# Kernel tuning notes

Hardware: AMD Instinct MI355X
Metric: run time of the kernel (lower is better)

Reference implementation:

```python
import jax, jax.numpy as jnp
import numpy as np

B, L, H, HEADS, DK = 256, 20, 128, 8, 16
NT, NR = 4, 4
CHILD, PARENT = 30001, 500
N1S, N1D, E1 = 50000, 20000, 300000
N2, E2 = 20000, 200000
T = B * L
N4D, E4 = 5000, 150000
EC2P = 8000
D2 = H // 2  # gamma=0.5 split for diachronic embedding


def _ln(x):
    m = jnp.mean(x, -1, keepdims=True)
    v = jnp.var(x, -1, keepdims=True)
    return (x - m) * jax.lax.rsqrt(v + 1e-5)


def _tmod(h, w, b):
    # temporal modulation with per-node diachronic params (activ='sin')
    return jnp.concatenate([h[..., :D2], h[..., D2:] * jnp.sin(w[..., D2:] + b[..., D2:])], -1)


def _dia(e, w, b, t):
    t = t[..., None].astype(e.dtype)
    return jnp.concatenate([e[..., :D2], e[..., D2:] * jnp.sin(w[..., D2:] * t + b[..., D2:])], -1)


def _typed(x, t, W):
    # type-conditioned linear: W [NT, in, out]; small NT -> compute all, select
    y = jnp.einsum('nh,tho->tno', x, W)
    return y[t, jnp.arange(x.shape[0])]


def _seg_softmax(s, seg, n):
    m = jax.ops.segment_max(s, seg, num_segments=n)
    m = jnp.where(jnp.isfinite(m), m, 0.0)
    ex = jnp.exp(s - m[seg])
    den = jax.ops.segment_sum(ex, seg, num_segments=n)
    return ex / jnp.maximum(den[seg], 1e-9)


def _htgt(src_h, src_t, tw, tb, eh, esrc, edst, etype, dst_h, dst_t, KW, QW, VW, OW, EW, mu):
    # relational multi-head attention on a bipartite block (HTGTLayer, pre_norm)
    nd = dst_h.shape[0]
    hs = _tmod(_ln(src_h), tw, tb)
    k = _typed(hs, src_t, KW).reshape(-1, HEADS, DK)
    v = _typed(hs, src_t, VW).reshape(-1, HEADS, DK)
    q = _typed(_ln(dst_h), dst_t, QW).reshape(nd, HEADS, DK)
    ke = k[esrc] + (eh @ EW).reshape(-1, HEADS, DK)
    score = (q[edst] * ke).sum(-1) * mu[etype] / np.float32(np.sqrt(DK))  # [E, HEADS]
    a = _seg_softmax(score, edst, nd)
    agg = jax.ops.segment_sum(a[..., None] * v[esrc], edst, num_segments=nd).reshape(nd, H)
    return _typed(agg, dst_t, OW) + dst_h


def _lstm(x, Wi, Wh, b):
    h0 = jnp.zeros((x.shape[0], H), x.dtype)
    def step(carry, xt):
        h, c = carry
        g = xt @ Wi + h @ Wh + b
        i, f, gg, o = jnp.split(g, 4, -1)
        c = jax.nn.sigmoid(f) * c + jax.nn.sigmoid(i) * jnp.tanh(gg)
        h = jax.nn.sigmoid(o) * jnp.tanh(c)
        return (h, c), h
    _, hs = jax.lax.scan(step, (h0, h0), jnp.swapaxes(x, 0, 1))
    return jnp.swapaxes(hs, 0, 1)


def _forward(seq, seq_ntype, dur, stime, etime, g1_nid, g1_ntype, g1_esrc, g1_edst, g1_etype, g1_ew,
             g2_src_sel, g2_esrc, g2_edst, g2_etype, g2_ew, tok_sel, g4_esrc, g4_edst, g4_etype, g4_ew,
             pe_p, pe_c, emb, hist_emb, edge_emb, dia_w, dia_b, t2v_w, t2v_b, exp_W, exp_b,
             lstm1_Wi, lstm1_Wh, lstm1_b, lstm2_Wi, lstm2_Wh, lstm2_b,
             convK, convQ, convV, convO, convE, convMu, ipW, iaW, skip):
    # ---- sequence module ----
    e0 = emb[seq]
    st = _dia(e0, dia_w[seq], dia_b[seq], stime)
    et = _dia(e0, dia_w[seq], dia_b[seq], etime)
    t = dur[..., None].astype(jnp.float32)
    tv = jnp.concatenate([t2v_w[:1] * t + t2v_b[:1], jnp.sin(t2v_w[1:] * t + t2v_b[1:])], -1)
    x = jax.nn.relu(jnp.concatenate([st, et, tv], -1) @ exp_W + exp_b)
    h1 = _lstm(x, lstm1_Wi, lstm1_Wh, lstm1_b)
    his = jnp.swapaxes(h1, 0, 1).reshape(T, H)  # packed (time-major) token states
    tok_id = jnp.swapaxes(seq, 0, 1).reshape(T)
    tok_nt = jnp.swapaxes(seq_ntype, 0, 1).reshape(T)
    # ---- conv1 (g2g) on block 1 ----
    sh1 = emb[g1_nid]
    xg = jax.nn.relu(_htgt(sh1, g1_ntype, dia_w[g1_nid], dia_b[g1_nid], edge_emb[g1_ew],
                           g1_esrc, g1_edst, g1_etype, sh1[:N1D], g1_ntype[:N1D],
                           convK[0], convQ[0], convV[0], convO[0], convE[0], convMu[0]))
    # ---- conv2 (g2s): graph nodes -> packed sequence tokens ----
    gnid2 = g1_nid[g2_src_sel]
    dst_h2 = xg[tok_sel] + his
    x2 = jax.nn.relu(_htgt(xg[g2_src_sel], g1_ntype[g2_src_sel], dia_w[gnid2], dia_b[gnid2], edge_emb[g2_ew],
                           g2_esrc, g2_edst, g2_etype, dst_h2, tok_nt,
                           convK[1], convQ[1], convV[1], convO[1], convE[1], convMu[1]))
    seq2 = jnp.swapaxes(x2.reshape(L, B, H), 0, 1)
    h2 = _lstm(seq2, lstm2_Wi, lstm2_Wh, lstm2_b)  # final seq_embed
    # ---- individual pooling (attn) + history push ----
    ent = jnp.swapaxes(h2, 0, 1).reshape(T, H)
    a = _typed(jnp.tanh(_typed(ent, tok_nt, ipW)), tok_nt, iaW)[:, 0]
    w = _seg_softmax(a, tok_id, CHILD)
    node_embed = jax.ops.segment_sum(w[:, None] * ent, tok_id, num_segments=CHILD)
    cnt = jax.ops.segment_sum(jnp.ones((T,), jnp.float32), tok_id, num_segments=CHILD)
    hist2 = jnp.where(cnt[:, None] > 0, node_embed, hist_emb)
    # ---- graph module: conv3, conv4 with skip-gated pull ----
    alpha = jax.nn.sigmoid(skip)[g1_ntype][:, None]
    x0 = emb[g1_nid] * alpha + hist2[g1_nid] * (1.0 - alpha)
    x3 = jax.nn.relu(_htgt(x0, g1_ntype, dia_w[g1_nid], dia_b[g1_nid], edge_emb[g1_ew],
                           g1_esrc, g1_edst, g1_etype, x0[:N1D], g1_ntype[:N1D],
                           convK[2], convQ[2], convV[2], convO[2], convE[2], convMu[2]))
    nid4 = g1_nid[:N1D]
    child_embed = _htgt(x3, g1_ntype[:N1D], dia_w[nid4], dia_b[nid4], edge_emb[g4_ew],
                        g4_esrc, g4_edst, g4_etype, x3[:N4D], g1_ntype[:N4D],
                        convK[3], convQ[3], convV[3], convO[3], convE[3], convMu[3])
    # ---- parent pooling (avg over c2p map) ----
    psum = jax.ops.segment_sum(child_embed[pe_c], pe_p, num_segments=PARENT)
    pcnt = jax.ops.segment_sum(jnp.ones((EC2P,), jnp.float32), pe_p, num_segments=PARENT)
    parent_embed = psum / jnp.maximum(pcnt, 1.0)[:, None]
    return (h2, child_embed, parent_embed)


def setup_inputs() -> dict:
    key = jax.random.key(0)
    ks = iter(jax.random.split(key, 64))
    def ri(shape, hi):
        return jax.random.randint(next(ks), shape, 0, hi, dtype=jnp.int32)
    def rn(shape, s=0.02):
        return jax.random.normal(next(ks), shape, dtype=jnp.float32) * s
    return dict(
        seq=ri((B, L), CHILD), seq_ntype=ri((B, L), NT), dur=ri((B, L), 40),
        stime=ri((B, L), 60), etime=ri((B, L), 60),
        g1_nid=ri((N1S,), CHILD), g1_ntype=ri((N1S,), NT),
        g1_esrc=ri((E1,), N1S), g1_edst=ri((E1,), N1D), g1_etype=ri((E1,), NR), g1_ew=ri((E1,), 50),
        g2_src_sel=ri((N2,), N1D), g2_esrc=ri((E2,), N2), g2_edst=ri((E2,), T),
        g2_etype=ri((E2,), NR), g2_ew=ri((E2,), 50),
        tok_sel=ri((T,), N1D),
        g4_esrc=ri((E4,), N1D), g4_edst=ri((E4,), N4D), g4_etype=ri((E4,), NR), g4_ew=ri((E4,), 50),
        pe_p=ri((EC2P,), PARENT), pe_c=ri((EC2P,), N4D),
        emb=rn((CHILD, H), 0.05), hist_emb=rn((CHILD, H), 0.05), edge_emb=rn((50, 32), 0.05),
        dia_w=rn((CHILD, H), 0.05), dia_b=rn((CHILD, H), 0.05),
        t2v_w=rn((16,), 0.1), t2v_b=rn((16,), 0.1),
        exp_W=rn((2 * H + 16, H)), exp_b=jnp.zeros((H,), jnp.float32),
        lstm1_Wi=rn((H, 4 * H)), lstm1_Wh=rn((H, 4 * H)), lstm1_b=jnp.zeros((4 * H,), jnp.float32),
        lstm2_Wi=rn((H, 4 * H)), lstm2_Wh=rn((H, 4 * H)), lstm2_b=jnp.zeros((4 * H,), jnp.float32),
        convK=rn((4, NT, H, H)), convQ=rn((4, NT, H, H)), convV=rn((4, NT, H, H)), convO=rn((4, NT, H, H)),
        convE=rn((4, 32, H)), convMu=jnp.ones((4, NR, HEADS), jnp.float32),
        ipW=rn((NT, H, H)), iaW=rn((NT, H, 1)), skip=jnp.ones((NT,), jnp.float32),
    )


def reference(seq, seq_ntype, dur, stime, etime, g1_nid, g1_ntype, g1_esrc, g1_edst, g1_etype, g1_ew,
              g2_src_sel, g2_esrc, g2_edst, g2_etype, g2_ew, tok_sel, g4_esrc, g4_edst, g4_etype, g4_ew,
              pe_p, pe_c, emb, hist_emb, edge_emb, dia_w, dia_b, t2v_w, t2v_b, exp_W, exp_b,
              lstm1_Wi, lstm1_Wh, lstm1_b, lstm2_Wi, lstm2_Wh, lstm2_b,
              convK, convQ, convV, convO, convE, convMu, ipW, iaW, skip):
    return _forward(seq, seq_ntype, dur, stime, etime, g1_nid, g1_ntype, g1_esrc, g1_edst, g1_etype, g1_ew,
                    g2_src_sel, g2_esrc, g2_edst, g2_etype, g2_ew, tok_sel, g4_esrc, g4_edst, g4_etype, g4_ew,
                    pe_p, pe_c, emb, hist_emb, edge_emb, dia_w, dia_b, t2v_w, t2v_b, exp_W, exp_b,
                    lstm1_Wi, lstm1_Wh, lstm1_b, lstm2_Wi, lstm2_Wh, lstm2_b,
                    convK, convQ, convV, convO, convE, convMu, ipW, iaW, skip)
```

## Files before the change

kernel.cpp:

```cpp
#include <hip/hip_runtime.h>
#include <math.h>

#define BB 256
#define LL 20
#define HH 128
#define NH 8
#define D2C 64
#define NTY 4
#define NRL 4
#define CHILDN 30001
#define PARENTN 500
#define N1SN 50000
#define N1DN 20000
#define E1N 300000
#define N2N 20000
#define E2N 200000
#define TT (BB*LL)
#define N4DN 5000
#define E4N 150000
#define EC2PN 8000

typedef __attribute__((ext_vector_type(8))) short bfrag;
typedef __attribute__((ext_vector_type(4))) float ffrag;

__device__ __forceinline__ unsigned fenc(float f){ unsigned u=__float_as_uint(f); return (u&0x80000000u)? ~u : (u|0x80000000u); }
__device__ __forceinline__ float fdec(unsigned u){ return (u&0x80000000u)? __uint_as_float(u^0x80000000u) : __uint_as_float(~u); }
__device__ __forceinline__ float sigfast(float x){ return 1.f/(1.f+__expf(-x)); }
__device__ __forceinline__ float tanhfast(float x){ float e = __expf(-2.f*x); return (1.f-e)/(1.f+e); }
__device__ __forceinline__ short f2bf(float f){
  unsigned u = __float_as_uint(f);
  unsigned r = u + 0x7FFFu + ((u>>16)&1u);
  return (short)(r>>16);
}

__global__ void k_init(float* hist2, float* cnt, unsigned* amax, float* aden,
                       float* psum, float* pcnt, int* cntall,
                       int* icnt1, int* icnt2, int* icnt3){
  int i = blockIdx.x*256 + threadIdx.x;
  if(i < CHILDN*HH) hist2[i] = 0.f;
  if(i < CHILDN){ cnt[i] = 0.f; aden[i] = 0.f; amax[i] = 0x007FFFFFu; }
  if(i < PARENTN*HH) psum[i] = 0.f;
  if(i < PARENTN) pcnt[i] = 0.f;
  if(i < 5*NTY) cntall[i] = 0;
  if(i < N1DN) icnt1[i] = 0;
  if(i < TT)   icnt2[i] = 0;
  if(i < N4DN) icnt3[i] = 0;
}

__global__ void k_sindia(const float* __restrict__ dia_w, const float* __restrict__ dia_b,
                         float* __restrict__ sdia){
  int i = blockIdx.x*256 + threadIdx.x;
  if(i >= CHILDN*64) return;
  int c = i >> 6, k = (i & 63) + 64;
  sdia[i] = __sinf(dia_w[(size_t)c*HH+k] + dia_b[(size_t)c*HH+k]);
}

__global__ __launch_bounds__(512) void k_featx2(const int* __restrict__ seq, const int* __restrict__ dur,
                        const int* __restrict__ stime, const int* __restrict__ etime,
                        const float* __restrict__ emb, const float* __restrict__ dia_w, const float* __restrict__ dia_b,
                        const float* __restrict__ t2v_w, const float* __restrict__ t2v_b,
                        const float* __restrict__ exp_W, const float* __restrict__ exp_b, float* __restrict__ xout){
  __shared__ float feat[32*273];
  int base = blockIdx.x*32;
  int j = threadIdx.x >> 4;
  int p = threadIdx.x & 15;
  int row = base + j;
  int node = seq[row];
  float ts = (float)stime[row], te = (float)etime[row];
  const float* ep = emb + (size_t)node*HH;
  float* fr = feat + j*273;
  int o0 = p*8;
  #pragma unroll
  for(int ii=0; ii<8; ii+=4){
    int o = o0 + ii;
    float4 e = *(const float4*)(ep + o);
    float4 st = e, et = e;
    if(o >= D2C){
      float4 w = *(const float4*)(dia_w + (size_t)node*HH + o);
      float4 b = *(const float4*)(dia_b + (size_t)node*HH + o);
      st.x = e.x*__sinf(w.x*ts+b.x); st.y = e.y*__sinf(w.y*ts+b.y);
      st.z = e.z*__sinf(w.z*ts+b.z); st.w = e.w*__sinf(w.w*ts+b.w);
      et.x = e.x*__sinf(w.x*te+b.x); et.y = e.y*__sinf(w.y*te+b.y);
      et.z = e.z*__sinf(w.z*te+b.z); et.w = e.w*__sinf(w.w*te+b.w);
    }
    fr[o] = st.x; fr[o+1] = st.y; fr[o+2] = st.z; fr[o+3] = st.w;
    fr[128+o] = et.x; fr[128+o+1] = et.y; fr[128+o+2] = et.z; fr[128+o+3] = et.w;
  }
  if(p == 0){
    float td = (float)dur[row];
    #pragma unroll
    for(int i=0;i<16;i++){
      float w = t2v_w[i], b = t2v_b[i];
      fr[256+i] = (i==0) ? (w*td + b) : __sinf(w*td + b);
    }
  }
  __syncthreads();
  int oc = (threadIdx.x & 31)*4;
  int jg = threadIdx.x >> 5;
  const float* f0 = feat + (jg*2)*273;
  const float* f1 = feat + (jg*2+1)*273;
  float4 a0 = {0,0,0,0}, a1 = {0,0,0,0};
  for(int k=0;k<272;k++){
    float4 w = *(const float4*)(exp_W + (size_t)k*HH + oc);
// ... 101 lines not shown
  if(threadIdx.x < NTY) h[threadIdx.x] = 0;
  __syncthreads();
  int nt = 0, r = 0;
  bool act = (i < TT);
  if(act){
    int b = i % BB, l = i / BB;
    tokid[i] = seq[b*LL+l];
    nt = seq_nt[b*LL+l];
    toknt[i] = nt;
    r = atomicAdd(&h[nt], 1);
  }
  __syncthreads();
  if(threadIdx.x < NTY && h[threadIdx.x] > 0)
    bs[threadIdx.x] = atomicAdd(&cnts[threadIdx.x], h[threadIdx.x]);
  __syncthreads();
  if(act) idxb[nt*TT + bs[nt] + r] = i;
}

__global__ void k_prep2scat(const int* __restrict__ sel, const int* __restrict__ g1_nid,
                            const int* __restrict__ g1_nt, int* __restrict__ gnid2,
                            int* __restrict__ cnts, int* __restrict__ idxb){
  __shared__ int h[NTY];
  __shared__ int bs[NTY];
  int i = blockIdx.x*256 + threadIdx.x;
  if(threadIdx.x < NTY) h[threadIdx.x] = 0;
  __syncthreads();
  int nt = 0, r = 0;
  bool act = (i < N2N);
  if(act){
    int s = sel[i];
    gnid2[i] = g1_nid[s];
    nt = g1_nt[s];
    r = atomicAdd(&h[nt], 1);
  }
  __syncthreads();
  if(threadIdx.x < NTY && h[threadIdx.x] > 0)
    bs[threadIdx.x] = atomicAdd(&cnts[threadIdx.x], h[threadIdx.x]);
  __syncthreads();
  if(act) idxb[nt*N2N + bs[nt] + r] = i;
}

__global__ void k_dst2(const int* tok_sel, const float* xg, const float* h1, float* dst2){
  int t = blockIdx.x; int o = threadIdx.x;
  int b = t % BB, l = t / BB;
  dst2[t*HH+o] = xg[tok_sel[t]*HH+o] + h1[(b*LL+l)*HH+o];
}

__global__ void k_x0(const int* nid, const int* ntype, const float* emb, const float* hist2,
                     const float* skip, float* srcbuf){
  int i = blockIdx.x; int o = threadIdx.x;
  float a = sigfast(skip[ntype[i]]);
  int nd = nid[i];
  srcbuf[i*HH+o] = emb[nd*HH+o]*a + hist2[nd*HH+o]*(1.f-a);
}

__global__ void k_scatter3(const int* __restrict__ types,
                           int* cnts1, int* idx1, int* cnts2, int* idx2, int* cnts3, int* idx3){
  __shared__ int h[3][NTY];
  __shared__ int bs[3][NTY];
  int i = blockIdx.x*256 + threadIdx.x;
  if(threadIdx.x < 3*NTY) (&h[0][0])[threadIdx.x] = 0;
  __syncthreads();
  int t = 0, r1 = 0, r2 = 0, r3 = 0;
  bool a1 = (i < N1SN), a2 = (i < N1DN), a3 = (i < N4DN);
  if(a1){
    t = types[i];
    r1 = atomicAdd(&h[0][t], 1);
    if(a2) r2 = atomicAdd(&h[1][t], 1);
    if(a3) r3 = atomicAdd(&h[2][t], 1);
  }
  __syncthreads();
  if(threadIdx.x < NTY){
    int ty = threadIdx.x;
    if(h[0][ty] > 0) bs[0][ty] = atomicAdd(&cnts1[ty], h[0][ty]);
    if(h[1][ty] > 0) bs[1][ty] = atomicAdd(&cnts2[ty], h[1][ty]);
    if(h[2][ty] > 0) bs[2][ty] = atomicAdd(&cnts3[ty], h[2][ty]);
  }
  __syncthreads();
  if(a1) idx1[t*N1SN + bs[0][t] + r1] = i;
  if(a2) idx2[t*N1DN + bs[1][t] + r2] = i;
  if(a3) idx3[t*N4DN + bs[2][t] + r3] = i;
}

__global__ void k_prepack(const float* convK, const float* convV, const float* convQ,
                          const float* convO, short* Wsw){
  int m = blockIdx.x;
  int fam = m >> 4;
  int lt = m & 15;
  const float* src = (fam==0?convK:fam==1?convV:fam==2?convQ:convO) + (size_t)lt*HH*HH;
  short* dst = Wsw + (size_t)m*16384;
  for(int s=0;s<64;s++){
    int i = threadIdx.x + 256*s;
    int j = i & 7, lane = (i>>3)&63, kc = (i>>9)&3, nt = i>>11;
    int k = kc*32 + (lane>>4)*8 + j;
    int n = nt*16 + (lane&15);
    dst[i] = f2bf(src[k*HH+n]);
  }
}

__global__ __launch_bounds__(256) void k_gemm_kvq(
    const float* __restrict__ Xs, const int* __restrict__ src_nid, const int* __restrict__ smap,
    const float* __restrict__ sdia,
    const int* __restrict__ idxs, const int* __restrict__ cnts_s, int stride_s,
    const bfrag* __restrict__ WK, const bfrag* __restrict__ WV, unsigned* __restrict__ KVp,
    const float* __restrict__ Xq, const int* __restrict__ qmap,
    const int* __restrict__ idxd, const int* __restrict__ cnts_d, int stride_d,
    const bfrag* __restrict__ WQ, float* __restrict__ Qbuf){
  __shared__ float xs[32*132];
  __shared__ float red[512];
  __shared__ float mean_s[32], inv_s[32];
  __shared__ int sid[32], nid[32], xrow[32];
  int t = blockIdx.y;
  int tid = threadIdx.x;
  int base = blockIdx.x * 32;
  if(blockIdx.z == 0){
    int cnt = cnts_s[t];
    if(base >= cnt || cnt == 0) return;
    int nn = min(32, cnt - base);
    const int* ids = idxs + (size_t)t*stride_s + base;
    if(tid < 32){
      int s_ = (tid < nn) ? ids[tid] : ids[0];
      sid[tid] = s_; nid[tid] = src_nid[s_];
      xrow[tid] = smap ? smap[s_] : s_;
    }
    __syncthreads();
    #pragma unroll
    for(int s=0;s<16;s++){
      int elem = tid + 256*s;
      int k = elem & 127, j = elem >> 7;
      xs[j*132 + k] = Xs[(size_t)xrow[j]*HH + k];
    }
    __syncthreads();
    {
      int j = tid >> 3, p = tid & 7;
      float sm=0.f, sq=0.f;
      const float* xr = xs + j*132 + p*16;
      #pragma unroll
      for(int i=0;i<16;i++){ float v = xr[i]; sm += v; sq += v*v; }
      red[j*8+p] = sm; red[256 + j*8+p] = sq;
    }
    __syncthreads();
    if(tid < 32){
      float sm=0.f, sq=0.f;
      #pragma unroll
      for(int p=0;p<8;p++){ sm += red[tid*8+p]; sq += red[256+tid*8+p]; }
      float mean = sm*(1.f/128.f);
      float var = sq*(1.f/128.f) - mean*mean;
      mean_s[tid] = mean;
      inv_s[tid] = 1.f/sqrtf(fmaxf(var,0.f)+1e-5f);
    }
    __syncthreads();
    #pragma unroll
    for(int s=0;s<16;s++){
      int elem = tid + 256*s;
      int k = elem & 127, j = elem >> 7;
      float v = (xs[j*132+k] - mean_s[j]) * inv_s[j];
      if(k >= D2C) v *= sdia[(size_t)nid[j]*64 + (k - D2C)];
      xs[j*132+k] = v;
    }
    __syncthreads();
    int lane = tid & 63, w = tid >> 6;
    int mt = w & 1, ng0 = (w>>1)*4;
    int arow = mt*16 + (lane & 15);
    int koff = (lane >> 4)*8;
    int tb = t*2048;
    ffrag aK[4], aV[4];
    #pragma unroll
    for(int i=0;i<4;i++){ aK[i] = (ffrag){0.f,0.f,0.f,0.f}; aV[i] = (ffrag){0.f,0.f,0.f,0.f}; }
    #pragma unroll
    for(int kc=0;kc<4;kc++){
      const float* ap = xs + arow*132 + kc*32 + koff;
      bfrag a;
      #pragma unroll
      for(int j=0;j<8;j++) a[j] = f2bf(ap[j]);
      #pragma unroll
      for(int nt=0;nt<4;nt++){
        int fi = tb + ((ng0+nt)*4 + kc)*64 + lane;
        bfrag bk = WK[fi];
        bfrag bv = WV[fi];
        aK[nt] = __builtin_amdgcn_mfma_f32_16x16x32_bf16(a, bk, aK[nt], 0, 0, 0);
        aV[nt] = __builtin_amdgcn_mfma_f32_16x16x32_bf16(a, bv, aV[nt], 0, 0, 0);
      }
    }
    int col0 = lane & 15;
    int rb = mt*16 + (lane>>4)*4;
    #pragma unroll
    for(int nt=0;nt<4;nt++){
      int col = (ng0+nt)*16 + col0;
      #pragma unroll
      for(int i=0;i<4;i++){
        int n = rb + i;
        if(n < nn){
          unsigned pk = (unsigned short)f2bf(aK[nt][i]);
          unsigned pv = (unsigned short)f2bf(aV[nt][i]);
          KVp[(size_t)sid[n]*HH + col] = (pv<<16) | pk;
        }
      }
    }
  } else {
    int cnt = cnts_d[t];
    if(base >= cnt || cnt == 0) return;
    int nn = min(32, cnt - base);
    const int* ids = idxd + (size_t)t*stride_d + base;
    if(tid < 32){
      int s_ = (tid < nn) ? ids[tid] : ids[0];
      sid[tid] = s_;
      xrow[tid] = qmap ? qmap[s_] : s_;
    }
    __syncthreads();
    #pragma unroll
    for(int s=0;s<16;s++){
      int elem = tid + 256*s;
      int k = elem & 127, j = elem >> 7;
      xs[j*132 + k] = Xq[(size_t)xrow[j]*HH + k];
    }
    __syncthreads();
    {
      int j = tid >> 3, p = tid & 7;
      float sm=0.f, sq=0.f;
      const float* xr = xs + j*132 + p*16;
      #pragma unroll
      for(int i=0;i<16;i++){ float v = xr[i]; sm += v; sq += v*v; }
      red[j*8+p] = sm; red[256 + j*8+p] = sq;
    }
    __syncthreads();
    if(tid < 32){
      float sm=0.f, sq=0.f;
      #pragma unroll
      for(int p=0;p<8;p++){ sm += red[tid*8+p]; sq += red[256+tid*8+p]; }
      float mean = sm*(1.f/128.f);
      float var = sq*(1.f/128.f) - mean*mean;
      mean_s[tid] = mean;
      inv_s[tid] = 1.f/sqrtf(fmaxf(var,0.f)+1e-5f);
    }
    __syncthreads();
    #pragma unroll
    for(int s=0;s<16;s++){
      int elem = tid + 256*s;
      int k = elem & 127, j = elem >> 7;
      xs[j*132+k] = (xs[j*132+k] - mean_s[j]) * inv_s[j];
    }
    __syncthreads();
    int lane = tid & 63, w = tid >> 6;
    int mt = w & 1, ng0 = (w>>1)*4;
    int arow = mt*16 + (lane & 15);
    int koff = (lane >> 4)*8;
    int tb = t*2048;
    ffrag acc[4];
    #pragma unroll
    for(int i=0;i<4;i++) acc[i] = (ffrag){0.f,0.f,0.f,0.f};
    #pragma unroll
    for(int kc=0;kc<4;kc++){
      const float* ap = xs + arow*132 + kc*32 + koff;
      bfrag a;
      #pragma unroll
      for(int j=0;j<8;j++) a[j] = f2bf(ap[j]);
      #pragma unroll
      for(int nt=0;nt<4;nt++){
        bfrag b = WQ[tb + ((ng0+nt)*4 + kc)*64 + lane];
        acc[nt] = __builtin_amdgcn_mfma_f32_16x16x32_bf16(a, b, acc[nt], 0, 0, 0);
      }
    }
    int col0 = lane & 15;
    int rb = mt*16 + (lane>>4)*4;
    #pragma unroll
    for(int nt=0;nt<4;nt++){
      int col = (ng0+nt)*16 + col0;
      #pragma unroll
      for(int i=0;i<4;i++){
        int n = rb + i;
        if(n < nn) Qbuf[(size_t)sid[n]*HH + col] = acc[nt][i];
      }
    }
  }
}

__global__ void k_gemm_t5(const float* X, const int* xmap, const int* idxb, const int* cnts, int stride,
                          const bfrag* W, const float* resid, const int* rmap, float* Y, float* Y2,
                          int relu){
  int t = blockIdx.y;
  int cnt = cnts[t];
  int base = blockIdx.x * 32;
  if(base >= cnt || cnt == 0) return;
  int nn = min(32, cnt - base);
  const int* ids = idxb + (size_t)t*stride + base;
  __shared__ float xs[32*132];
  __shared__ int sid[32], xrow[32], rrow[32];
  int tid = threadIdx.x;
  if(tid < 32){
    int s_ = (tid < nn) ? ids[tid] : ids[0];
    sid[tid] = s_;
    xrow[tid] = xmap ? xmap[s_] : s_;
    rrow[tid] = rmap ? rmap[s_] : s_;
  }
  __syncthreads();
  #pragma unroll
  for(int s=0;s<16;s++){
    int elem = tid + 256*s;
    int k = elem & 127, j = elem >> 7;
    xs[j*132 + k] = X[(size_t)xrow[j]*HH + k];
  }
  __syncthreads();
  int lane = tid & 63, w = tid >> 6;
  int mt = w & 1, ng0 = (w>>1)*4;
  int arow = mt*16 + (lane & 15);
  int koff = (lane >> 4)*8;
  int tb = t*2048;
  ffrag acc[4];
  #pragma unroll
  for(int i=0;i<4;i++) acc[i] = (ffrag){0.f,0.f,0.f,0.f};
  #pragma unroll
  for(int kc=0;kc<4;kc++){
    const float* ap = xs + arow*132 + kc*32 + koff;
    bfrag a;
    #pragma unroll
    for(int j=0;j<8;j++) a[j] = f2bf(ap[j]);
    #pragma unroll
    for(int nt=0;nt<4;nt++){
      bfrag b = W[tb + ((ng0+nt)*4 + kc)*64 + lane];
      acc[nt] = __builtin_amdgcn_mfma_f32_16x16x32_bf16(a, b, acc[nt], 0, 0, 0);
    }
  }
  int col0 = lane & 15;
  int rb = mt*16 + (lane>>4)*4;
  #pragma unroll
  for(int nt=0;nt<4;nt++){
    int col = (ng0+nt)*16 + col0;
    #pragma unroll
    for(int i=0;i<4;i++){
      int n = rb + i;
      if(n < nn){
        size_t r = (size_t)sid[n]*HH + col;
        float v = acc[nt][i];
        if(resid){
          v += resid[(size_t)rrow[n]*HH + col];
          if(relu) v = fmaxf(v, 0.f);
        }
        Y[r] = v;
        if(Y2) Y2[r] = v;
      }
    }
  }
}

__global__ void k_edge_tab4(const float* edge_emb, const float* convE, float* EW2all){
  int r = blockIdx.x; int layer = blockIdx.y; int o = threadIdx.x;
  const float* EWp = convE + (size_t)layer*32*HH;
  float acc = 0.f;
  for(int j=0;j<32;j++) acc += edge_emb[r*32+j]*EWp[j*HH+o];
  EW2all[((size_t)layer*50 + r)*HH + o] = acc;
}

__global__ void k_hist_dst(const int* edst, int E, int* cnt){
  int e = blockIdx.x*256 + threadIdx.x;
  if(e < E) atomicAdd(&cnt[edst[e]], 1);
}
__global__ void k_scan3(const int* c1, int n1, int* r1, int* u1,
                        const int* c2, int n2, int* r2, int* u2,
                        const int* c3, int n3, int* r3, int* u3){
  __shared__ int tsum[1024];
  const int* cnt; int n; int* row_ptr; int* cursor;
  if(blockIdx.x == 0){ cnt=c1; n=n1; row_ptr=r1; cursor=u1; }
  else if(blockIdx.x == 1){ cnt=c2; n=n2; row_ptr=r2; cursor=u2; }
  else { cnt=c3; n=n3; row_ptr=r3; cursor=u3; }
  int tid = threadIdx.x;
  int per = (n + 1023) / 1024;
  int start = tid*per; int end = min(start+per, n);
  int s = 0;
  for(int i=start;i<end;i++) s += cnt[i];
  tsum[tid] = s; __syncthreads();
  for(int off=1;off<1024;off<<=1){
    int v = (tid>=off) ? tsum[tid-off] : 0;
    __syncthreads();
    tsum[tid] += v;
    __syncthreads();
  }
  int run = (tid==0) ? 0 : tsum[tid-1];
  for(int i=start;i<end;i++){ row_ptr[i]=run; cursor[i]=run; run += cnt[i]; }
  if(end == n) row_ptr[n] = run;
}
__global__ void k_fillperm(const int* edst, const int* esrc, const int* ew, const int* ety,
                           int E, int* cursor, int2* meta){
  int e = blockIdx.x*256 + threadIdx.x;
// ... 149 lines not shown
                              hipStream_t stream){
  const int* seq     = (const int*)d_in[0];
  const int* seq_nt  = (const int*)d_in[1];
  const int* dur     = (const int*)d_in[2];
  const int* stime   = (const int*)d_in[3];
  const int* etime   = (const int*)d_in[4];
  const int* g1_nid  = (const int*)d_in[5];
  const int* g1_nt   = (const int*)d_in[6];
  const int* g1_esrc = (const int*)d_in[7];
  const int* g1_edst = (const int*)d_in[8];
  const int* g1_ety  = (const int*)d_in[9];
  const int* g1_ew   = (const int*)d_in[10];
  const int* g2_sel  = (const int*)d_in[11];
  const int* g2_esrc = (const int*)d_in[12];
  const int* g2_edst = (const int*)d_in[13];
  const int* g2_ety  = (const int*)d_in[14];
  const int* g2_ew   = (const int*)d_in[15];
  const int* tok_sel = (const int*)d_in[16];
  const int* g4_esrc = (const int*)d_in[17];
  const int* g4_edst = (const int*)d_in[18];
  const int* g4_ety  = (const int*)d_in[19];
  const int* g4_ew   = (const int*)d_in[20];
  const int* pe_p    = (const int*)d_in[21];
  const int* pe_c    = (const int*)d_in[22];
  const float* emb     = (const float*)d_in[23];
  const float* hist_emb= (const float*)d_in[24];
  const float* edge_emb= (const float*)d_in[25];
  const float* dia_w   = (const float*)d_in[26];
  const float* dia_b   = (const float*)d_in[27];
  const float* t2v_w   = (const float*)d_in[28];
  const float* t2v_b   = (const float*)d_in[29];
  const float* exp_W   = (const float*)d_in[30];
  const float* exp_b   = (const float*)d_in[31];
  const float* l1Wi    = (const float*)d_in[32];
  const float* l1Wh    = (const float*)d_in[33];
  const float* l1b     = (const float*)d_in[34];
  const float* l2Wi    = (const float*)d_in[35];
  const float* l2Wh    = (const float*)d_in[36];
  const float* l2b     = (const float*)d_in[37];
  const float* convK   = (const float*)d_in[38];
  const float* convQ   = (const float*)d_in[39];
  const float* convV   = (const float*)d_in[40];
  const float* convO   = (const float*)d_in[41];
  const float* convE   = (const float*)d_in[42];
  const float* convMu  = (const float*)d_in[43];
  const float* ipW     = (const float*)d_in[44];
  const float* iaW     = (const float*)d_in[45];
  const float* skip    = (const float*)d_in[46];
  float* outp = (float*)d_out;

  char* wsp = (char*)d_ws;
  size_t off = 0;
  auto A = [&](size_t nbytes)->char*{ char* p = wsp+off; off += (nbytes+255)&~(size_t)255; return p; };
  float*    srcbuf = (float*)   A((size_t)N1SN*HH*4);
  unsigned* KVp    = (unsigned*)A((size_t)N1SN*HH*4);
  float*    Qbuf   = (float*)   A((size_t)N1DN*HH*4);
  float*    Abuf   = (float*)   A((size_t)N1DN*HH*4);
  float*    xbuf   = (float*)   A((size_t)TT*HH*4);
  float*    gpre   = (float*)   A((size_t)TT*512*4);
  float*    h1     = (float*)   A((size_t)TT*HH*4);
  float*    dst2   = (float*)   A((size_t)TT*HH*4);
  float*    xg     = (float*)   A((size_t)N1DN*HH*4);
  float*    x2     = (float*)   A((size_t)TT*HH*4);
  float*    h2f    = (float*)   A((size_t)TT*HH*4);
  float*    hist2  = (float*)   A((size_t)CHILDN*HH*4);
  float*    cnt    = (float*)   A((size_t)CHILDN*4);
  float*    abuf   = (float*)   A((size_t)TT*4);
  unsigned* amax   = (unsigned*)A((size_t)CHILDN*4);
  float*    aden   = (float*)   A((size_t)CHILDN*4);
  float*    x3     = (float*)   A((size_t)N1DN*HH*4);
  float*    cef    = (float*)   A((size_t)N4DN*HH*4);
  float*    psum   = (float*)   A((size_t)PARENTN*HH*4);
  float*    pcnt   = (float*)   A((size_t)PARENTN*4);
  float*    sdia   = (float*)   A((size_t)CHILDN*64*4);
  int*      tokid  = (int*)     A((size_t)TT*4);
  int*      toknt  = (int*)     A((size_t)TT*4);
  int*      gnid2  = (int*)     A((size_t)N2N*4);
  int*      idxS1  = (int*)     A((size_t)NTY*N1SN*4);
  int*      idxS2  = (int*)     A((size_t)NTY*N1DN*4);
  int*      idxS3  = (int*)     A((size_t)NTY*N2N*4);
  int*      idxS4  = (int*)     A((size_t)NTY*TT*4);
  int*      idxS5  = (int*)     A((size_t)NTY*N4DN*4);
  int*      cntall = (int*)     A((size_t)5*NTY*4);
  float*    EW2all = (float*)   A((size_t)4*50*HH*4);
  short*    Wsw    = (short*)   A((size_t)64*16384*2);
  int*      g1row  = (int*)     A((size_t)(N1DN+1)*4);
  int2*     g1meta = (int2*)    A((size_t)E1N*8);
  int*      g2row  = (int*)     A((size_t)(TT+1)*4);
  int2*     g2meta = (int2*)    A((size_t)E2N*8);
  int*      g4row  = (int*)     A((size_t)(N4DN+1)*4);
  int2*     g4meta = (int2*)    A((size_t)E4N*8);
  int*      icnt1  = (int*)     A((size_t)(N1DN+1)*4);
  int*      icur1  = (int*)     A((size_t)(N1DN+1)*4);
  int*      icnt2  = (int*)     A((size_t)(TT+1)*4);
  int*      icur2  = (int*)     A((size_t)(TT+1)*4);
  int*      icnt3  = (int*)     A((size_t)(N4DN+1)*4);
  int*      icur3  = (int*)     A((size_t)(N4DN+1)*4);
  if(off > ws_size) return;

  auto run_conv = [&](const float* src_X, const int* src_nid, const int* srcmap, int nsrc,
                      const int* idx_src, int* cnt_src, int stride_src,
                      const float* q_X, const int* q_map,
                      const float* resid_X, const int* r_map, int ndst,
                      const int* idx_dst, int* cnt_dst, int stride_dst,
                      const int* rowp, const int2* meta,
                      int layer, float* outbuf, float* out2, int relu){
    const bfrag* WB = (const bfrag*)Wsw;
    const bfrag* WK = WB + (size_t)( 0 + layer*4)*2048;
    const bfrag* WV = WB + (size_t)(16 + layer*4)*2048;
    const bfrag* WQ = WB + (size_t)(32 + layer*4)*2048;
    const bfrag* WO = WB + (size_t)(48 + layer*4)*2048;
    const float* MU  = convMu + (size_t)layer*NRL*NH;
    const float* EW2 = EW2all + (size_t)layer*50*HH;
    int gx = max((nsrc+31)/32, (ndst+31)/32);
    dim3 gkvq(gx, NTY, 2);
    k_gemm_kvq<<<gkvq, 256, 0, stream>>>(src_X, src_nid, srcmap, sdia,
                                         idx_src, cnt_src, stride_src, WK, WV, KVp,
                                         q_X, q_map, idx_dst, cnt_dst, stride_dst, WQ, Qbuf);
    k_attn_fused8<<<ndst, HH, 0, stream>>>(rowp, meta, KVp, Qbuf, EW2, MU, Abuf);
    dim3 gq((ndst+31)/32, NTY);
    k_gemm_t5<<<gq, 256, 0, stream>>>(Abuf, (const int*)nullptr, idx_dst, cnt_dst, stride_dst, WO,
                                      resid_X, r_map, outbuf, out2, relu);
  };

  k_init<<<(CHILDN*HH+255)/256, 256, 0, stream>>>(hist2, cnt, amax, aden, psum, pcnt, cntall,
                                                  icnt1, icnt2, icnt3);
  k_sindia<<<(CHILDN*64+255)/256, 256, 0, stream>>>(dia_w, dia_b, sdia);
  k_prepack<<<64, 256, 0, stream>>>(convK, convV, convQ, convO, Wsw);
  k_edge_tab4<<<dim3(50,4), HH, 0, stream>>>(edge_emb, convE, EW2all);
  k_scatter3<<<(N1SN+255)/256, 256, 0, stream>>>(g1_nt, cntall+0*NTY, idxS1,
                                                 cntall+1*NTY, idxS2, cntall+4*NTY, idxS5);
  k_tokprep<<<(TT+255)/256, 256, 0, stream>>>(seq, seq_nt, tokid, toknt, cntall+3*NTY, idxS4);
  k_prep2scat<<<(N2N+255)/256, 256, 0, stream>>>(g2_sel, g1_nid, g1_nt, gnid2, cntall+2*NTY, idxS3);
  k_hist_dst<<<(E1N+255)/256, 256, 0, stream>>>(g1_edst, E1N, icnt1);
  k_hist_dst<<<(E2N+255)/256, 256, 0, stream>>>(g2_edst, E2N, icnt2);
  k_hist_dst<<<(E4N+255)/256, 256, 0, stream>>>(g4_edst, E4N, icnt3);
  k_scan3<<<3, 1024, 0, stream>>>(icnt1, N1DN, g1row, icur1,
                                  icnt2, TT,   g2row, icur2,
                                  icnt3, N4DN, g4row, icur3);
  k_fillperm<<<(E1N+255)/256, 256, 0, stream>>>(g1_edst, g1_esrc, g1_ew, g1_ety, E1N, icur1, g1meta);
  k_fillperm<<<(E2N+255)/256, 256, 0, stream>>>(g2_edst, g2_esrc, g2_ew, g2_ety, E2N, icur2, g2meta);
  k_fillperm<<<(E4N+255)/256, 256, 0, stream>>>(g4_edst, g4_esrc, g4_ew, g4_ety, E4N, icur3, g4meta);

  k_featx2<<<TT/32, 512, 0, stream>>>(seq, dur, stime, etime, emb, dia_w, dia_b, t2v_w, t2v_b, exp_W, exp_b, xbuf);
  k_xwi2<<<(TT+15)/16, 256, 0, stream>>>(xbuf, l1Wi, l1b, gpre, TT, 0);
  k_lstm_fused<<<BB, 512, 0, stream>>>(gpre, l1Wh, h1, (float*)nullptr);

  run_conv(emb, g1_nid, g1_nid, N1SN, idxS1, cntall+0*NTY, N1SN,
           emb, g1_nid,
           emb, g1_nid, N1DN, idxS2, cntall+1*NTY, N1DN,
           g1row, g1meta, 0, xg, (float*)nullptr, 1);

  k_dst2<<<TT, HH, 0, stream>>>(tok_sel, xg, h1, dst2);
  run_conv(xg, gnid2, g2_sel, N2N, idxS3, cntall+2*NTY, N2N,
           dst2, (const int*)nullptr,
           dst2, (const int*)nullptr, TT, idxS4, cntall+3*NTY, TT,
           g2row, g2meta, 1, x2, (float*)nullptr, 1);

  k_xwi2<<<(TT+15)/16, 256, 0, stream>>>(x2, l2Wi, l2b, gpre, TT, 1);
  k_lstm_fused<<<BB, 512, 0, stream>>>(gpre, l2Wh, h2f, outp);

  k_tokatt<<<TT, HH, 0, stream>>>(h2f, toknt, ipW, iaW, abuf, amax, tokid);
  k_tokexp<<<(TT+255)/256, 256, 0, stream>>>(tokid, abuf, amax, aden, cnt);
  k_tokagg<<<TT, HH, 0, stream>>>(tokid, abuf, aden, h2f, hist2);
  k_histfix<<<CHILDN, HH, 0, stream>>>(cnt, hist_emb, hist2);

  k_x0<<<N1SN, HH, 0, stream>>>(g1_nid, g1_nt, emb, hist2, skip, srcbuf);
  run_conv(srcbuf, g1_nid, (const int*)nullptr, N1SN, idxS1, cntall+0*NTY, N1SN,
           srcbuf, (const int*)nullptr,
           srcbuf, (const int*)nullptr, N1DN, idxS2, cntall+1*NTY, N1DN,
           g1row, g1meta, 2, x3, (float*)nullptr, 1);

  run_conv(x3, g1_nid, (const int*)nullptr, N1DN, idxS2, cntall+1*NTY, N1DN,
           x3, (const int*)nullptr,
           x3, (const int*)nullptr, N4DN, idxS5, cntall+4*NTY, N4DN,
           g4row, g4meta, 3, cef, outp + (size_t)TT*HH, 0);

  k_peagg<<<EC2PN, HH, 0, stream>>>(pe_p, pe_c, cef, psum, pcnt);
  k_parent<<<PARENTN, HH, 0, stream>>>(psum, pcnt, outp + (size_t)TT*HH + (size_t)N4DN*HH);
}
```

Before: 777.2 us.

## Compact typed GEMM grids with precomputed tile descriptors and vectorised loads

Adds a single-block kernel that builds a compact list of 32-row tile descriptors per conv configuration from the per-type counts. The KVQ and output GEMMs then launch exactly over those tiles instead of a max-sized grid per type with many early-exit blocks. The change also merges the K/V and Q code paths, replaces the shared-memory layernorm reduction with wave shuffles, and uses float4 row gathers. The cost is an extra tiny serial launch and a descriptor indirection in each block.

```diff
diff --git a/kernel.cpp b/kernel.cpp
--- a/kernel.cpp
+++ b/kernel.cpp
@@ -19,6 +19,7 @@
 #define N4DN 5000
 #define E4N 150000
 #define EC2PN 8000
+#define TDSTRIDE 2304
 
 typedef __attribute__((ext_vector_type(8))) short bfrag;
 typedef __attribute__((ext_vector_type(4))) float ffrag;
@@ -286,6 +287,40 @@
   if(a3) idx3[t*N4DN + bs[2][t] + r3] = i;
 }
 
+__global__ void k_mktiles(const int* __restrict__ cntall, int* __restrict__ tdesc, int* __restrict__ tcnt){
+  __shared__ int start[3][2][NTY];
+  if(threadIdx.x == 0){
+    const int srcg[3] = {0,2,1};
+    const int dstg[3] = {1,3,4};
+    for(int c=0;c<3;c++){
+      int acc = 0;
+      for(int z=0;z<2;z++){
+        int g = (z==0) ? srcg[c] : dstg[c];
+        int zacc = 0;
+        for(int t=0;t<NTY;t++){
+          start[c][z][t] = acc;
+          int tiles = (cntall[g*NTY+t]+31)>>5;
+          acc += tiles; zacc += tiles;
+        }
+        tcnt[c*2+z] = zacc;
+      }
+    }
+  }
+  __syncthreads();
+  const int srcg[3] = {0,2,1};
+  const int dstg[3] = {1,3,4};
+  for(int c=0;c<3;c++){
+    for(int z=0;z<2;z++){
+      int g = (z==0) ? srcg[c] : dstg[c];
+      for(int t=0;t<NTY;t++){
+        int tiles = (cntall[g*NTY+t]+31)>>5;
+        for(int i=threadIdx.x; i<tiles; i+=blockDim.x)
+          tdesc[c*TDSTRIDE + start[c][z][t] + i] = (int)(((unsigned)z<<31) | ((unsigned)t<<28) | (unsigned)(i<<5));
+      }
+    }
+  }
+}
+
 __global__ void k_prepack(const float* convK, const float* convV, const float* convQ,
                           const float* convO, short* Wsw){
   int m = blockIdx.x;
@@ -303,6 +338,7 @@
 }
 
 __global__ __launch_bounds__(256) void k_gemm_kvq(
+    const int* __restrict__ tdesc, const int* __restrict__ tcnt,
     const float* __restrict__ Xs, const int* __restrict__ src_nid, const int* __restrict__ smap,
     const float* __restrict__ sdia,
     const int* __restrict__ idxs, const int* __restrict__ cnts_s, int stride_s,
@@ -311,49 +347,55 @@
     const int* __restrict__ idxd, const int* __restrict__ cnts_d, int stride_d,
     const bfrag* __restrict__ WQ, float* __restrict__ Qbuf){
   __shared__ float xs[32*132];
-  __shared__ float red[512];
   __shared__ float mean_s[32], inv_s[32];
   __shared__ int sid[32], nid[32], xrow[32];
-  int t = blockIdx.y;
+  int ntk = tcnt[0], ntq = tcnt[1];
+  int bid = blockIdx.x;
+  if(bid >= ntk + ntq) return;
+  unsigned ud = (unsigned)tdesc[bid];
+  int isQ = ud >> 31;
+  int t = (ud >> 28) & 7;
+  int base = ud & 0x0FFFFFFF;
   int tid = threadIdx.x;
-  int base = blockIdx.x * 32;
-  if(blockIdx.z == 0){
-    int cnt = cnts_s[t];
-    if(base >= cnt || cnt == 0) return;
-    int nn = min(32, cnt - base);
-    const int* ids = idxs + (size_t)t*stride_s + base;
-    if(tid < 32){
-      int s_ = (tid < nn) ? ids[tid] : ids[0];
-      sid[tid] = s_; nid[tid] = src_nid[s_];
-      xrow[tid] = smap ? smap[s_] : s_;
-    }
-    __syncthreads();
-    #pragma unroll
-    for(int s=0;s<16;s++){
-      int elem = tid + 256*s;
-      int k = elem & 127, j = elem >> 7;
-      xs[j*132 + k] = Xs[(size_t)xrow[j]*HH + k];
-    }
-    __syncthreads();
-    {
-      int j = tid >> 3, p = tid & 7;
-      float sm=0.f, sq=0.f;
-      const float* xr = xs + j*132 + p*16;
-      #pragma unroll
-      for(int i=0;i<16;i++){ float v = xr[i]; sm += v; sq += v*v; }
-      red[j*8+p] = sm; red[256 + j*8+p] = sq;
-    }
-    __syncthreads();
-    if(tid < 32){
-      float sm=0.f, sq=0.f;
-      #pragma unroll
-      for(int p=0;p<8;p++){ sm += red[tid*8+p]; sq += red[256+tid*8+p]; }
+  int cnt = isQ ? cnts_d[t] : cnts_s[t];
+  if(base >= cnt) return;
+  int nn = min(32, cnt - base);
+  const float* X = isQ ? Xq : Xs;
+  const int* map = isQ ? qmap : smap;
+  const int* ids = (isQ ? idxd + (size_t)t*stride_d : idxs + (size_t)t*stride_s) + base;
+  if(tid < 32){
+    int s_ = (tid < nn) ? ids[tid] : ids[0];
+    sid[tid] = s_;
+    if(!isQ) nid[tid] = src_nid[s_];
+    xrow[tid] = map ? map[s_] : s_;
+  }
+  __syncthreads();
+  #pragma unroll
+  for(int s=0;s<4;s++){
+    int e4 = tid + 256*s;
+    int j = e4 >> 5, c4 = (e4 & 31)*4;
+    *(float4*)&xs[j*132 + c4] = *(const float4*)&X[(size_t)xrow[j]*HH + c4];
+  }
+  __syncthreads();
+  {
+    int wid = tid >> 6, lane = tid & 63;
+    int row = wid*8 + (lane>>3), p = lane & 7;
+    const float* xr = xs + row*132 + p*16;
+    float sm=0.f, sq=0.f;
+    #pragma unroll
+    for(int i=0;i<16;i++){ float v = xr[i]; sm += v; sq += v*v; }
+    sm += __shfl_xor(sm, 1, 64); sq += __shfl_xor(sq, 1, 64);
+    sm += __shfl_xor(sm, 2, 64); sq += __shfl_xor(sq, 2, 64);
+    sm += __shfl_xor(sm, 4, 64); sq += __shfl_xor(sq, 4, 64);
+    if(p == 0){
       float mean = sm*(1.f/128.f);
       float var = sq*(1.f/128.f) - mean*mean;
-      mean_s[tid] = mean;
-      inv_s[tid] = 1.f/sqrtf(fmaxf(var,0.f)+1e-5f);
-    }
-    __syncthreads();
+      mean_s[row] = mean;
+      inv_s[row] = 1.f/sqrtf(fmaxf(var,0.f)+1e-5f);
+    }
+  }
+  __syncthreads();
+  if(!isQ){
     #pragma unroll
     for(int s=0;s<16;s++){
       int elem = tid + 256*s;
@@ -362,12 +404,21 @@
       if(k >= D2C) v *= sdia[(size_t)nid[j]*64 + (k - D2C)];
       xs[j*132+k] = v;
     }
-    __syncthreads();
-    int lane = tid & 63, w = tid >> 6;
-    int mt = w & 1, ng0 = (w>>1)*4;
-    int arow = mt*16 + (lane & 15);
-    int koff = (lane >> 4)*8;
-    int tb = t*2048;
+  } else {
+    #pragma unroll
+    for(int s=0;s<16;s++){
+      int elem = tid + 256*s;
+      int k = elem & 127, j = elem >> 7;
+      xs[j*132+k] = (xs[j*132+k] - mean_s[j]) * inv_s[j];
+    }
+  }
+  __syncthreads();
+  int lane = tid & 63, w = tid >> 6;
+  int mt = w & 1, ng0 = (w>>1)*4;
+  int arow = mt*16 + (lane & 15);
+  int koff = (lane >> 4)*8;
+  int tb = t*2048;
+  if(!isQ){
     ffrag aK[4], aV[4];
     #pragma unroll
     for(int i=0;i<4;i++){ aK[i] = (ffrag){0.f,0.f,0.f,0.f}; aV[i] = (ffrag){0.f,0.f,0.f,0.f}; }
@@ -402,54 +453,6 @@
       }
     }
   } else {
-    int cnt = cnts_d[t];
-    if(base >= cnt || cnt == 0) return;
-    int nn = min(32, cnt - base);
-    const int* ids = idxd + (size_t)t*stride_d + base;
-    if(tid < 32){
-      int s_ = (tid < nn) ? ids[tid] : ids[0];
-      sid[tid] = s_;
-      xrow[tid] = qmap ? qmap[s_] : s_;
-    }
-    __syncthreads();
-    #pragma unroll
-    for(int s=0;s<16;s++){
-      int elem = tid + 256*s;
-      int k = elem & 127, j = elem >> 7;
-      xs[j*132 + k] = Xq[(size_t)xrow[j]*HH + k];
-    }
-    __syncthreads();
-    {
-      int j = tid >> 3, p = tid & 7;
-      float sm=0.f, sq=0.f;
-      const float* xr = xs + j*132 + p*16;
-      #pragma unroll
-      for(int i=0;i<16;i++){ float v = xr[i]; sm += v; sq += v*v; }
-      red[j*8+p] = sm; red[256 + j*8+p] = sq;
-    }
-    __syncthreads();
-    if(tid < 32){
-      float sm=0.f, sq=0.f;
-      #pragma unroll
-      for(int p=0;p<8;p++){ sm += red[tid*8+p]; sq += red[256+tid*8+p]; }
-      float mean = sm*(1.f/128.f);
-      float var = sq*(1.f/128.f) - mean*mean;
-      mean_s[tid] = mean;
-      inv_s[tid] = 1.f/sqrtf(fmaxf(var,0.f)+1e-5f);
-    }
-    __syncthreads();
-    #pragma unroll
-    for(int s=0;s<16;s++){
-      int elem = tid + 256*s;
-      int k = elem & 127, j = elem >> 7;
-      xs[j*132+k] = (xs[j*132+k] - mean_s[j]) * inv_s[j];
-    }
-    __syncthreads();
-    int lane = tid & 63, w = tid >> 6;
-    int mt = w & 1, ng0 = (w>>1)*4;
-    int arow = mt*16 + (lane & 15);
-    int koff = (lane >> 4)*8;
-    int tb = t*2048;
     ffrag acc[4];
     #pragma unroll
     for(int i=0;i<4;i++) acc[i] = (ffrag){0.f,0.f,0.f,0.f};
@@ -479,30 +482,34 @@
   }
 }
 
-__global__ void k_gemm_t5(const float* X, const int* xmap, const int* idxb, const int* cnts, int stride,
-                          const bfrag* W, const float* resid, const int* rmap, float* Y, float* Y2,
-                          int relu){
-  int t = blockIdx.y;
+__global__ __launch_bounds__(256) void k_gemm_t5(
+    const int* __restrict__ tdesc, const int* __restrict__ tcnt,
+    const float* X, const int* idxb, const int* cnts, int stride,
+    const bfrag* W, const float* resid, const int* rmap, float* Y, float* Y2,
+    int relu){
+  __shared__ float xs[32*132];
+  __shared__ int sid[32], rrow[32];
+  int ntk = tcnt[0], ntq = tcnt[1];
+  if(blockIdx.x >= ntq) return;
+  unsigned ud = (unsigned)tdesc[ntk + blockIdx.x];
+  int t = (ud >> 28) & 7;
+  int base = ud & 0x0FFFFFFF;
   int cnt = cnts[t];
-  int base = blockIdx.x * 32;
-  if(base >= cnt || cnt == 0) return;
+  if(base >= cnt) return;
   int nn = min(32, cnt - base);
   const int* ids = idxb + (size_t)t*stride + base;
-  __shared__ float xs[32*132];
-  __shared__ int sid[32], xrow[32], rrow[32];
   int tid = threadIdx.x;
   if(tid < 32){
     int s_ = (tid < nn) ? ids[tid] : ids[0];
     sid[tid] = s_;
-    xrow[tid] = xmap ? xmap[s_] : s_;
     rrow[tid] = rmap ? rmap[s_] : s_;
   }
   __syncthreads();
   #pragma unroll
-  for(int s=0;s<16;s++){
-    int elem = tid + 256*s;
-    int k = elem & 127, j = elem >> 7;
-    xs[j*132 + k] = X[(size_t)xrow[j]*HH + k];
+  for(int s=0;s<4;s++){
+    int e4 = tid + 256*s;
+    int j = e4 >> 5, c4 = (e4 & 31)*4;
+    *(float4*)&xs[j*132 + c4] = *(const float4*)&X[(size_t)sid[j]*HH + c4];
   }
   __syncthreads();
   int lane = tid & 63, w = tid >> 6;
@@ -818,6 +825,8 @@
   int*      idxS4  = (int*)     A((size_t)NTY*TT*4);
   int*      idxS5  = (int*)     A((size_t)NTY*N4DN*4);
   int*      cntall = (int*)     A((size_t)5*NTY*4);
+  int*      tdesc  = (int*)     A((size_t)3*TDSTRIDE*4);
+  int*      tcnt   = (int*)     A((size_t)8*4);
   float*    EW2all = (float*)   A((size_t)4*50*HH*4);
   short*    Wsw    = (short*)   A((size_t)64*16384*2);
   int*      g1row  = (int*)     A((size_t)(N1DN+1)*4);
@@ -834,7 +843,8 @@
   int*      icur3  = (int*)     A((size_t)(N4DN+1)*4);
   if(off > ws_size) return;
 
-  auto run_conv = [&](const float* src_X, const int* src_nid, const int* srcmap, int nsrc,
+  auto run_conv = [&](int cfg, int gkvq, int gq,
+                      const float* src_X, const int* src_nid, const int* srcmap,
                       const int* idx_src, int* cnt_src, int stride_src,
                       const float* q_X, const int* q_map,
                       const float* resid_X, const int* r_map, int ndst,
@@ -848,14 +858,13 @@
     const bfrag* WO = WB + (size_t)(48 + layer*4)*2048;
     const float* MU  = convMu + (size_t)layer*NRL*NH;
     const float* EW2 = EW2all + (size_t)layer*50*HH;
-    int gx = max((nsrc+31)/32, (ndst+31)/32);
-    dim3 gkvq(gx, NTY, 2);
-    k_gemm_kvq<<<gkvq, 256, 0, stream>>>(src_X, src_nid, srcmap, sdia,
+    const int* td = tdesc + (size_t)cfg*TDSTRIDE;
+    const int* tc = tcnt + cfg*2;
+    k_gemm_kvq<<<gkvq, 256, 0, stream>>>(td, tc, src_X, src_nid, srcmap, sdia,
                                          idx_src, cnt_src, stride_src, WK, WV, KVp,
                                          q_X, q_map, idx_dst, cnt_dst, stride_dst, WQ, Qbuf);
     k_attn_fused8<<<ndst, HH, 0, stream>>>(rowp, meta, KVp, Qbuf, EW2, MU, Abuf);
-    dim3 gq((ndst+31)/32, NTY);
-    k_gemm_t5<<<gq, 256, 0, stream>>>(Abuf, (const int*)nullptr, idx_dst, cnt_dst, stride_dst, WO,
+    k_gemm_t5<<<gq, 256, 0, stream>>>(td, tc, Abuf, idx_dst, cnt_dst, stride_dst, WO,
                                       resid_X, r_map, outbuf, out2, relu);
   };
 
@@ -868,6 +877,7 @@
                                                  cntall+1*NTY, idxS2, cntall+4*NTY, idxS5);
   k_tokprep<<<(TT+255)/256, 256, 0, stream>>>(seq, seq_nt, tokid, toknt, cntall+3*NTY, idxS4);
   k_prep2scat<<<(N2N+255)/256, 256, 0, stream>>>(g2_sel, g1_nid, g1_nt, gnid2, cntall+2*NTY, idxS3);
+  k_mktiles<<<1, 256, 0, stream>>>(cntall, tdesc, tcnt);
   k_hist_dst<<<(E1N+255)/256, 256, 0, stream>>>(g1_edst, E1N, icnt1);
   k_hist_dst<<<(E2N+255)/256, 256, 0, stream>>>(g2_edst, E2N, icnt2);
   k_hist_dst<<<(E4N+255)/256, 256, 0, stream>>>(g4_edst, E4N, icnt3);
@@ -882,13 +892,22 @@
   k_xwi2<<<(TT+15)/16, 256, 0, stream>>>(xbuf, l1Wi, l1b, gpre, TT, 0);
   k_lstm_fused<<<BB, 512, 0, stream>>>(gpre, l1Wh, h1, (float*)nullptr);
 
-  run_conv(emb, g1_nid, g1_nid, N1SN, idxS1, cntall+0*NTY, N1SN,
+  const int GKVQ_A = (N1SN+N1DN)/32 + 8;
+  const int GKVQ_B = (N2N+TT)/32 + 8;
+  const int GKVQ_C = (N1DN+N4DN)/32 + 8;
+  const int GQ_A   = (N1DN+31)/32 + 4;
+  const int GQ_B   = (TT+31)/32 + 4;
+  const int GQ_C   = (N4DN+31)/32 + 4;
+
+  run_conv(0, GKVQ_A, GQ_A,
+           emb, g1_nid, g1_nid, idxS1, cntall+0*NTY, N1SN,
            emb, g1_nid,
            emb, g1_nid, N1DN, idxS2, cntall+1*NTY, N1DN,
            g1row, g1meta, 0, xg, (float*)nullptr, 1);
 
   k_dst2<<<TT, HH, 0, stream>>>(tok_sel, xg, h1, dst2);
-  run_conv(xg, gnid2, g2_sel, N2N, idxS3, cntall+2*NTY, N2N,
+  run_conv(1, GKVQ_B, GQ_B,
+           xg, gnid2, g2_sel, idxS3, cntall+2*NTY, N2N,
            dst2, (const int*)nullptr,
            dst2, (const int*)nullptr, TT, idxS4, cntall+3*NTY, TT,
            g2row, g2meta, 1, x2, (float*)nullptr, 1);
@@ -902,12 +921,14 @@
   k_histfix<<<CHILDN, HH, 0, stream>>>(cnt, hist_emb, hist2);
 
   k_x0<<<N1SN, HH, 0, stream>>>(g1_nid, g1_nt, emb, hist2, skip, srcbuf);
-  run_conv(srcbuf, g1_nid, (const int*)nullptr, N1SN, idxS1, cntall+0*NTY, N1SN,
+  run_conv(0, GKVQ_A, GQ_A,
+           srcbuf, g1_nid, (const int*)nullptr, idxS1, cntall+0*NTY, N1SN,
            srcbuf, (const int*)nullptr,
            srcbuf, (const int*)nullptr, N1DN, idxS2, cntall+1*NTY, N1DN,
            g1row, g1meta, 2, x3, (float*)nullptr, 1);
 
-  run_conv(x3, g1_nid, (const int*)nullptr, N1DN, idxS2, cntall+1*NTY, N1DN,
+  run_conv(2, GKVQ_C, GQ_C,
+           x3, g1_nid, (const int*)nullptr, idxS2, cntall+1*NTY, N1DN,
            x3, (const int*)nullptr,
            x3, (const int*)nullptr, N4DN, idxS5, cntall+4*NTY, N4DN,
            g4row, g4meta, 3, cef, outp + (size_t)TT*HH, 0);
```

After: 798.2 us. 1.03x slower.
